# Kernel optimization log

Hardware: AMD Instinct MI355X
Metric: run time of the kernel (lower is better)

## Reference

```python
import jax, jax.numpy as jnp
import numpy as np

N = 50000   # nodes
E = 500000  # edges
NEG_SLOPE = 0.2


def _edge_softmax(e, dst, n):
    # softmax over edges grouped by destination node (DGL edge_softmax)
    m = jax.ops.segment_max(e, dst, num_segments=n)          # [N,H]
    ex = jnp.exp(e - m[dst])
    s = jax.ops.segment_sum(ex, dst, num_segments=n)
    return ex / s[dst]


def _gat(h, W, al, ar, b, src, dst, heads, d, Wres=None, act=True):
    # DGL GATConv (eval mode, no dropout)
    n = h.shape[0]
    feat = (h @ W).reshape(n, heads, d)                      # [N,H,D]
    el = jnp.sum(feat * al[None], axis=-1)                   # [N,H]
    er = jnp.sum(feat * ar[None], axis=-1)                   # [N,H]
    e = jax.nn.leaky_relu(el[src] + er[dst], NEG_SLOPE)      # [E,H]
    a = _edge_softmax(e, dst, n)                             # [E,H]
    rst = jax.ops.segment_sum(feat[src] * a[..., None], dst, num_segments=n)  # [N,H,D]
    if Wres is not None:
        res = (h @ Wres).reshape(n, heads, d)
    else:
        res = h.reshape(n, heads, d)                         # identity residual (in == heads*d)
    rst = rst + res + b.reshape(1, heads, d)
    if act:
        rst = jax.nn.elu(rst)
    return rst.reshape(n, heads * d)


def _bn(x, g, b, m, v):
    # BatchNorm1d in eval mode
    return (x - m) * g * jax.lax.rsqrt(v + 1e-5) + b


def setup_inputs() -> dict:
    key = jax.random.key(0)
    ks = jax.random.split(key, 40)
    rn = lambda i, s: jax.random.normal(ks[i], s, jnp.float32) * 0.1
    inp = dict(
        node_feats=jax.random.normal(ks[0], (N, 128), jnp.float32),
        edge_feats=jax.random.normal(ks[1], (E, 64), jnp.float32),
        src=jax.random.randint(ks[2], (E,), 0, N, jnp.int32),
        dst=jax.random.randint(ks[3], (E,), 0, N, jnp.int32),
        # GAT layer 0: 128 -> 8 heads x 16
        W0=rn(4, (128, 128)), al0=rn(5, (8, 16)), ar0=rn(6, (8, 16)), b0=rn(7, (128,)),
        g0=1.0 + rn(8, (128,)), bt0=rn(9, (128,)), m0=rn(10, (128,)),
        v0=1.0 + 0.1 * jax.random.uniform(ks[11], (128,), jnp.float32),
        # GAT layer 1: 128 -> 8 heads x 8 (residual projection)
        W1=rn(12, (128, 64)), al1=rn(13, (8, 8)), ar1=rn(14, (8, 8)), b1=rn(15, (64,)),
        Wres1=rn(16, (128, 64)),
        g1=1.0 + rn(17, (64,)), bt1=rn(18, (64,)), m1=rn(19, (64,)),
        v1=1.0 + 0.1 * jax.random.uniform(ks[20], (64,), jnp.float32),
        # GAT layer 2: 64 -> 1 head x 32 (residual projection, no activation)
        W2=rn(21, (64, 32)), al2=rn(22, (1, 32)), ar2=rn(23, (1, 32)), b2=rn(24, (32,)),
        Wres2=rn(25, (64, 32)),
        g2=1.0 + rn(26, (32,)), bt2=rn(27, (32,)), m2=rn(28, (32,)),
        v2=1.0 + 0.1 * jax.random.uniform(ks[29], (32,), jnp.float32),
        # edge projection 64 -> 128
        We=rn(30, (64, 128)), be=rn(31, (128,)),
        # edge classifier: 192 -> 32 -> 16 -> 2
        Wc1=rn(32, (192, 32)), bc1=rn(33, (32,)),
        Wc2=rn(34, (32, 16)), bc2=rn(35, (16,)),
        Wc3=rn(36, (16, 2)), bc3=rn(37, (2,)),
    )
    return inp


def reference(node_feats, edge_feats, src, dst,
              W0, al0, ar0, b0, g0, bt0, m0, v0,
              W1, al1, ar1, b1, Wres1, g1, bt1, m1, v1,
              W2, al2, ar2, b2, Wres2, g2, bt2, m2, v2,
              We, be, Wc1, bc1, Wc2, bc2, Wc3, bc3):
    h = _bn(_gat(node_feats, W0, al0, ar0, b0, src, dst, 8, 16), g0, bt0, m0, v0)
    h = _bn(_gat(h, W1, al1, ar1, b1, src, dst, 8, 8, Wres1), g1, bt1, m1, v1)
    h = _bn(_gat(h, W2, al2, ar2, b2, src, dst, 1, 32, Wres2, act=False), g2, bt2, m2, v2)
    ef = jax.nn.relu(edge_feats @ We + be)                   # [E,128]
    rep = jnp.concatenate([h[src], h[dst], ef], axis=1)      # [E,192]
    z = jax.nn.relu(rep @ Wc1 + bc1)
    z = jax.nn.relu(z @ Wc2 + bc2)
    return z @ Wc3 + bc3                                     # [E,2]
```

## Files before the change

kernel.cpp:

```cpp
#include <hip/hip_runtime.h>
#include <cfloat>
#include <math.h>

#define NEG_SLOPE 0.2f

typedef short short8 __attribute__((ext_vector_type(8)));
typedef short short4v __attribute__((ext_vector_type(4)));
typedef float f32x4 __attribute__((ext_vector_type(4)));

__device__ __forceinline__ short f2bf(float x) {
    unsigned u = __float_as_uint(x);
    u += 0x7fffu + ((u >> 16) & 1u);
    return (short)(u >> 16);
}
__device__ __forceinline__ float bf2f(unsigned short s) {
    return __uint_as_float((unsigned)s << 16);
}

__device__ __forceinline__ void lds_fence() {
    __asm__ __volatile__("s_waitcnt lgkmcnt(0)" ::: "memory");
}


__global__ void count_deg_k(const int* __restrict__ dst, int* __restrict__ deg, int E) {
    int i = blockIdx.x * 256 + threadIdx.x;
    if (i < E) atomicAdd(&deg[dst[i]], 1);
}

__global__ void scan_k(const int* __restrict__ deg, int* __restrict__ off, int n) {
    __shared__ int part[1024];
    int tid = threadIdx.x;
    int chunk = (n + 1023) >> 10;
    int beg = tid * chunk;
    int end = min(beg + chunk, n);
    int s = 0;
    for (int i = beg; i < end; ++i) s += deg[i];
    part[tid] = s;
    __syncthreads();
    for (int d = 1; d < 1024; d <<= 1) {
        int v = (tid >= d) ? part[tid - d] : 0;
        __syncthreads();
        part[tid] += v;
        __syncthreads();
    }
    int run = (tid > 0) ? part[tid - 1] : 0;
    for (int i = beg; i < end; ++i) { off[i] = run; run += deg[i]; }
    if (tid == 1023) off[n] = part[1023];
}

__global__ void scatter_k(const int* __restrict__ src, const int* __restrict__ dst,
                          const int* __restrict__ off, int* __restrict__ cur,
                          int* __restrict__ srcp, int E) {
    int i = blockIdx.x * 256 + threadIdx.x;
    if (i >= E) return;
    int d = dst[i];
    int p = off[d] + atomicAdd(&cur[d], 1);
    srcp[p] = src[i];
}


__global__ void conv_w_k(const float* __restrict__ We, const float* __restrict__ Wc1p,
                         const float* __restrict__ Wc2,
                         short* __restrict__ WeTg, short* __restrict__ Wc1Tg,
                         short* __restrict__ Wc2Tg) {
    int t = blockIdx.x * 256 + threadIdx.x;
    if (t < 64 * 128) { int k = t >> 7, n = t & 127; WeTg[n * 64 + k] = f2bf(We[t]); }
    if (t < 128 * 32) { int k = t >> 5, n = t & 31; Wc1Tg[n * 128 + k] = f2bf(Wc1p[t]); }
    if (t < 32 * 16)  { int k = t >> 4, n = t & 15; Wc2Tg[n * 32 + k] = f2bf(Wc2[t]); }
}


template<int K, int OUT, bool B16>
__global__ __launch_bounds__(256) void gemm2_k(const float* __restrict__ A,
                                               const float* __restrict__ B1, float* __restrict__ C1,
                                               const float* __restrict__ B2, float* __restrict__ C2,
                                               short* __restrict__ C1b, int nrows) {
    constexpr int CPT  = (OUT >= 64) ? 8 : 4;
    constexpr int CG   = OUT / CPT;
    constexpr int TY   = 256 / CG;
    constexpr int ROWS = TY * 4;
    constexpr int KT   = (K < 32) ? K : 32;
    constexpr int KTP  = KT + 4;

    __shared__ float As[ROWS * KTP];
    __shared__ float Bs[KT * OUT];

    const float* B = blockIdx.y ? B2 : B1;
    float*       C = blockIdx.y ? C2 : C1;

    int t = threadIdx.x;
    int tx = t % CG, ty = t / CG;
    int row0 = blockIdx.x * ROWS;

    float acc[4][CPT];
#pragma unroll
    for (int r = 0; r < 4; ++r)
#pragma unroll
        for (int c = 0; c < CPT; ++c) acc[r][c] = 0.f;

    for (int k0 = 0; k0 < K; k0 += KT) {
        __syncthreads();
#pragma unroll
        for (int i = t; i < ROWS * (KT / 4); i += 256) {
            int row = i / (KT / 4), c4 = i % (KT / 4);
            float4 v = {0.f, 0.f, 0.f, 0.f};
            if (row0 + row < nrows)
                v = *(const float4*)&A[(size_t)(row0 + row) * K + k0 + c4 * 4];
            *(float4*)&As[row * KTP + c4 * 4] = v;
        }
#pragma unroll
        for (int i = t; i < KT * (OUT / 4); i += 256) {
            int k = i / (OUT / 4), c4 = i % (OUT / 4);
            *(float4*)&Bs[k * OUT + c4 * 4] = *(const float4*)&B[(size_t)(k0 + k) * OUT + c4 * 4];
        }
        __syncthreads();

#pragma unroll
        for (int kk4 = 0; kk4 < KT / 4; ++kk4) {
            float4 a4[4];
#pragma unroll
            for (int r = 0; r < 4; ++r)
                a4[r] = *(const float4*)&As[(ty * 4 + r) * KTP + kk4 * 4];
#pragma unroll
            for (int j = 0; j < 4; ++j) {
                int kk = kk4 * 4 + j;
                float4 b4[CPT / 4];
#pragma unroll
                for (int c = 0; c < CPT / 4; ++c)
                    b4[c] = *(const float4*)&Bs[kk * OUT + tx * CPT + c * 4];
#pragma unroll
                for (int r = 0; r < 4; ++r) {
                    float a = ((const float*)&a4[r])[j];
#pragma unroll
                    for (int c = 0; c < CPT / 4; ++c) {
                        acc[r][c * 4 + 0] = fmaf(a, b4[c].x, acc[r][c * 4 + 0]);
                        acc[r][c * 4 + 1] = fmaf(a, b4[c].y, acc[r][c * 4 + 1]);
                        acc[r][c * 4 + 2] = fmaf(a, b4[c].z, acc[r][c * 4 + 2]);
                        acc[r][c * 4 + 3] = fmaf(a, b4[c].w, acc[r][c * 4 + 3]);
                    }
                }
            }
        }
    }

#pragma unroll
    for (int r = 0; r < 4; ++r) {
        int row = row0 + ty * 4 + r;
        if (row < nrows) {
#pragma unroll
            for (int c = 0; c < CPT / 4; ++c) {
                float4 v = {acc[r][c * 4 + 0], acc[r][c * 4 + 1], acc[r][c * 4 + 2], acc[r][c * 4 + 3]};
                *(float4*)&C[(size_t)row * OUT + tx * CPT + c * 4] = v;
            }
            if (B16 && blockIdx.y == 0) {
                if constexpr (CPT == 8) {
                    short8 s;
#pragma unroll
                    for (int c = 0; c < 8; ++c) s[c] = f2bf(acc[r][c]);
                    *(short8*)&C1b[(size_t)row * OUT + tx * CPT] = s;
                } else {
                    short4v s;
#pragma unroll
                    for (int c = 0; c < 4; ++c) s[c] = f2bf(acc[r][c]);
                    *(short4v*)&C1b[(size_t)row * OUT + tx * CPT] = s;
                }
            }
        }
    }
}


template<int H, int D>
__global__ void elr_k(const float* __restrict__ feat, const float* __restrict__ al,
                      const float* __restrict__ ar, float* __restrict__ el,
                      float* __restrict__ er, int n) {
    int i = blockIdx.x * 256 + threadIdx.x;
    if (i >= n * H) return;
    int h = i % H;
    const float* f = feat + (size_t)(i / H) * (H * D) + h * D;
    float sl = 0.f, sr = 0.f;
#pragma unroll
    for (int d = 0; d < D; ++d) {
        sl = fmaf(f[d], al[h * D + d], sl);
        sr = fmaf(f[d], ar[h * D + d], sr);
    }
    el[i] = sl; er[i] = sr;
}


template<int H, int D, bool ACT>
__global__ __launch_bounds__(256) void gat_node2_k(
    const int* __restrict__ off, const int* __restrict__ srcp,
    const float* __restrict__ el, const float* __restrict__ er,
    const short* __restrict__ featb,
    const float* __restrict__ res, const float* __restrict__ bias,
    const float* __restrict__ bg, const float* __restrict__ bb,
    const float* __restrict__ bm, const float* __restrict__ bv,
    float* __restrict__ hout, int N) {
    constexpr int HD = H * D;
    constexpr bool PAIR = (HD > 64);
    constexpr int CH = 64 / H;
    int wv_ = threadIdx.x >> 6;
    int lane = threadIdx.x & 63;
    int n = blockIdx.x * 4 + wv_;
    if (n >= N) return;
    int beg = off[n], end = off[n + 1];

    int hh = lane % H;
    int cc = lane / H;
    float ern = er[(size_t)n * H + hh];

    int k0 = PAIR ? 2 * lane : lane;
    int h0 = k0 / D; if (h0 > H - 1) h0 = H - 1;

    float acc0 = 0.f, acc1 = 0.f, svp = 0.f;

    for (int i0 = beg; i0 < end; i0 += CH) {
        int iw = i0 + cc;
        float wv = 0.f;
        int sidx = 0;
        if (iw < end) {
            sidx = srcp[iw];
            float x = el[(size_t)sidx * H + hh] + ern;
            x = x > 0.f ? x : NEG_SLOPE * x;
            wv = __expf(x);
        }
        svp += wv;
        int lim = min(end - i0, CH);
        for (int r = 0; r < lim; ++r) {
            int sl = r * H + h0;
            float w0 = __shfl(wv, sl, 64);
            int s    = __shfl(sidx, sl, 64);
            if constexpr (PAIR) {
                ushort2 uv = *(const ushort2*)&featb[(size_t)s * HD + k0];
                acc0 = fmaf(w0, bf2f(uv.x), acc0);
                acc1 = fmaf(w0, bf2f(uv.y), acc1);
            } else {
                if (lane < HD)
                    acc0 = fmaf(w0, bf2f((unsigned short)featb[(size_t)s * HD + k0]), acc0);
            }
        }
    }
#pragma unroll
    for (int mm = H; mm < 64; mm <<= 1) svp += __shfl_xor(svp, mm, 64);
    bool has_edges = end > beg;
    float inv0 = has_edges ? 1.f / __shfl(svp, h0, 64) : 0.f;

    if constexpr (PAIR) {
        float2 rs = *(const float2*)&res[(size_t)n * HD + k0];
        float2 bi = *(const float2*)&bias[k0];
        float2 gm = *(const float2*)&bm[k0];
        float2 gv = *(const float2*)&bv[k0];
        float2 gg = *(const float2*)&bg[k0];
        float2 gb = *(const float2*)&bb[k0];
        float x0 = acc0 * inv0 + rs.x + bi.x;
        float x1 = acc1 * inv0 + rs.y + bi.y;
        if (ACT) { x0 = x0 > 0.f ? x0 : expm1f(x0); x1 = x1 > 0.f ? x1 : expm1f(x1); }
        float2 o;
        o.x = (x0 - gm.x) * (gg.x * rsqrtf(gv.x + 1e-5f)) + gb.x;
        o.y = (x1 - gm.y) * (gg.y * rsqrtf(gv.y + 1e-5f)) + gb.y;
        *(float2*)&hout[(size_t)n * HD + k0] = o;
    } else {
        if (lane < HD) {
            int k = k0;
            float x = acc0 * inv0 + res[(size_t)n * HD + k] + bias[k];
            if (ACT) x = x > 0.f ? x : expm1f(x);
            hout[(size_t)n * HD + k] = (x - bm[k]) * (bg[k] * rsqrtf(bv[k] + 1e-5f)) + bb[k];
        }
    }
}


__global__ __launch_bounds__(256) void edge_cls_k(
    const float* __restrict__ u1, const float* __restrict__ u2,
    const float* __restrict__ edf,
    const int* __restrict__ src, const int* __restrict__ dst,
    const short* __restrict__ WeTg, const float* __restrict__ be,
    const short* __restrict__ Wc1Tg, const float* __restrict__ bc1,
    const short* __restrict__ Wc2Tg, const float* __restrict__ bc2,
    const float* __restrict__ Wc3, const float* __restrict__ bc3,
    float* __restrict__ out, int E) {
    __shared__ short efA[4][16 * 136];
    __shared__ short z1A[4][16 * 40];
    __shared__ float z2A[4][16 * 20];

    int t = threadIdx.x;
    int w = t >> 6, lane = t & 63;
    int m = lane & 15, q = lane >> 4;
    short* efW = efA[w];
    short* z1W = z1A[w];
    float* z2W = z2A[w];

    int tiles = (E + 15) >> 4;
    int gw = blockIdx.x * 4 + w;
    int W  = gridDim.x * 4;

    float bc2h = bc2[m];
    float bc30 = bc3[0], bc31 = bc3[1];

    auto ldrow = [&](int tl, float4& a, float4& b, float4& c, float4& d) {
        int em = tl * 16 + m;
        const float* rp = edf + (size_t)(em < E ? em : E - 1) * 64;
        a = *(const float4*)(rp + q * 8);
        b = *(const float4*)(rp + q * 8 + 4);
        c = *(const float4*)(rp + 32 + q * 8);
        d = *(const float4*)(rp + 32 + q * 8 + 4);
    };
    auto ldu = [&](int tl, float (&ua)[2][4], float (&ub)[2][4]) {
#pragma unroll
        for (int r = 0; r < 4; ++r) {
            int e = tl * 16 + q * 4 + r;
            int ec = e < E ? e : E - 1;
            int s = src[ec], d = dst[ec];
            ua[0][r] = u1[(size_t)s * 32 + m];
            ua[1][r] = u1[(size_t)s * 32 + 16 + m];
            ub[0][r] = u2[(size_t)d * 32 + m];
            ub[1][r] = u2[(size_t)d * 32 + 16 + m];
        }
    };

    int tile = gw;
    float4 p0 = {0,0,0,0}, p1 = p0, p2 = p0, p3 = p0;
    float u1g[2][4], u2g[2][4];
    if (tile < tiles) { ldrow(tile, p0, p1, p2, p3); ldu(tile, u1g, u2g); }

    for (; tile < tiles; tile += W) {
        float4 c0 = p0, c1 = p1, c2 = p2, c3 = p3;
        int tn = tile + W;
        if (tn < tiles) ldrow(tn, p0, p1, p2, p3);

        int e0w = tile * 16;

        short8 A0, A1;
        A0[0] = f2bf(c0.x); A0[1] = f2bf(c0.y); A0[2] = f2bf(c0.z); A0[3] = f2bf(c0.w);
        A0[4] = f2bf(c1.x); A0[5] = f2bf(c1.y); A0[6] = f2bf(c1.z); A0[7] = f2bf(c1.w);
        A1[0] = f2bf(c2.x); A1[1] = f2bf(c2.y); A1[2] = f2bf(c2.z); A1[3] = f2bf(c2.w);
        A1[4] = f2bf(c3.x); A1[5] = f2bf(c3.y); A1[6] = f2bf(c3.z); A1[7] = f2bf(c3.w);

#pragma unroll
        for (int nt = 0; nt < 8; ++nt) {
            int col = nt * 16 + m;
            float bias = be[col];
            f32x4 acc = {bias, bias, bias, bias};
            short8 b0 = *(const short8*)&WeTg[col * 64 + q * 8];
            short8 b1 = *(const short8*)&WeTg[col * 64 + 32 + q * 8];
            acc = __builtin_amdgcn_mfma_f32_16x16x32_bf16(A0, b0, acc, 0, 0, 0);
            acc = __builtin_amdgcn_mfma_f32_16x16x32_bf16(A1, b1, acc, 0, 0, 0);
#pragma unroll
            for (int r = 0; r < 4; ++r)
                efW[(q * 4 + r) * 136 + col] = f2bf(fmaxf(acc[r], 0.f));
        }
        lds_fence();

        short8 Az[4];
#pragma unroll
        for (int kt = 0; kt < 4; ++kt)
            Az[kt] = *(const short8*)&efW[m * 136 + kt * 32 + q * 8];
#pragma unroll
        for (int nt = 0; nt < 2; ++nt) {
            int col = nt * 16 + m;
            float bias = bc1[col];
            f32x4 acc = {bias, bias, bias, bias};
#pragma unroll
            for (int kt = 0; kt < 4; ++kt) {
                short8 b = *(const short8*)&Wc1Tg[col * 128 + kt * 32 + q * 8];
                acc = __builtin_amdgcn_mfma_f32_16x16x32_bf16(Az[kt], b, acc, 0, 0, 0);
            }
#pragma unroll
            for (int r = 0; r < 4; ++r) {
                float z = acc[r] + u1g[nt][r] + u2g[nt][r];
                z1W[(q * 4 + r) * 40 + col] = f2bf(fmaxf(z, 0.f));
            }
        }
        lds_fence();

        if (tn < tiles) ldu(tn, u1g, u2g);

        {
            short8 Az1 = *(const short8*)&z1W[m * 40 + q * 8];
            short8 Bz  = *(const short8*)&Wc2Tg[m * 32 + q * 8];
            f32x4 acc = {bc2h, bc2h, bc2h, bc2h};
            acc = __builtin_amdgcn_mfma_f32_16x16x32_bf16(Az1, Bz, acc, 0, 0, 0);
#pragma unroll
            for (int r = 0; r < 4; ++r)
                z2W[(q * 4 + r) * 20 + m] = fmaxf(acc[r], 0.f);
        }
        lds_fence();

        if (lane < 16) {
            int e = lane;
            int eg = e0w + e;
            if (eg < E) {
                float a0 = bc30, a1 = bc31;
#pragma unroll
                for (int k = 0; k < 16; ++k) {
                    float z = z2W[e * 20 + k];
                    a0 = fmaf(z, Wc3[k * 2], a0);
                    a1 = fmaf(z, Wc3[k * 2 + 1], a1);
                }
                float2 o = {a0, a1};
                *(float2*)&out[(size_t)eg * 2] = o;
            }
        }
        lds_fence();
    }
}


extern "C" void kernel_launch(void* const* d_in, const int* in_sizes, int n_in,
                              void* d_out, int out_size, void* d_ws, size_t ws_size,
                              hipStream_t stream) {
    const float* node_feats = (const float*)d_in[0];
    const float* edge_feats = (const float*)d_in[1];
    const int*   src  = (const int*)d_in[2];
    const int*   dst  = (const int*)d_in[3];
    const float* W0   = (const float*)d_in[4];
    const float* al0  = (const float*)d_in[5];
    const float* ar0  = (const float*)d_in[6];
    const float* b0   = (const float*)d_in[7];
    const float* g0   = (const float*)d_in[8];
    const float* bt0  = (const float*)d_in[9];
    const float* m0   = (const float*)d_in[10];
    const float* v0   = (const float*)d_in[11];
    const float* W1   = (const float*)d_in[12];
    const float* al1  = (const float*)d_in[13];
    const float* ar1  = (const float*)d_in[14];
    const float* b1   = (const float*)d_in[15];
    const float* Wr1  = (const float*)d_in[16];
    const float* g1   = (const float*)d_in[17];
    const float* bt1  = (const float*)d_in[18];
    const float* m1   = (const float*)d_in[19];
    const float* v1   = (const float*)d_in[20];
    const float* W2   = (const float*)d_in[21];
    const float* al2  = (const float*)d_in[22];
    const float* ar2  = (const float*)d_in[23];
    const float* b2   = (const float*)d_in[24];
    const float* Wr2  = (const float*)d_in[25];
    const float* g2   = (const float*)d_in[26];
    const float* bt2  = (const float*)d_in[27];
    const float* v2m  = (const float*)d_in[28];
    const float* v2v  = (const float*)d_in[29];
    const float* We   = (const float*)d_in[30];
    const float* be   = (const float*)d_in[31];
    const float* Wc1  = (const float*)d_in[32];
    const float* bc1  = (const float*)d_in[33];
    const float* Wc2  = (const float*)d_in[34];
    const float* bc2  = (const float*)d_in[35];
    const float* Wc3  = (const float*)d_in[36];
    const float* bc3  = (const float*)d_in[37];
    float* out = (float*)d_out;

    const int N = in_sizes[0] / 128;
    const int E = in_sizes[2];

    char* p = (char*)d_ws;
    auto alloc = [&](size_t bytes) -> void* {
        void* r = (void*)p;
        p += (bytes + 255) & ~(size_t)255;
        return r;
    };
    int*   deg  = (int*)alloc((size_t)N * 4);
    int*   cur  = (int*)alloc((size_t)N * 4);
    int*   off  = (int*)alloc((size_t)(N + 1) * 4);
    int*   srcp = (int*)alloc((size_t)E * 4);
    float* feat = (float*)alloc((size_t)N * 128 * 4);
    short* featb= (short*)alloc((size_t)N * 128 * 2);
    float* resf = (float*)alloc((size_t)N * 64 * 4);
    float* h1   = (float*)alloc((size_t)N * 128 * 4);
    float* h2   = (float*)alloc((size_t)N * 64 * 4);
    float* h3   = (float*)alloc((size_t)N * 32 * 4);
    float* el   = (float*)alloc((size_t)N * 8 * 4);
    float* er   = (float*)alloc((size_t)N * 8 * 4);
    short* WeTg = (short*)alloc((size_t)128 * 64 * 2);
    short* Wc1Tg= (short*)alloc((size_t)32 * 128 * 2);
    short* Wc2Tg= (short*)alloc((size_t)16 * 32 * 2);
    float* u1   = h1;
    float* u2   = h1 + (size_t)N * 32;

    hipMemsetAsync(deg, 0, (size_t)N * 4, stream);
    hipMemsetAsync(cur, 0, (size_t)N * 4, stream);

    int eb = (E + 255) / 256;
    count_deg_k<<<eb, 256, 0, stream>>>(dst, deg, E);
    scan_k<<<1, 1024, 0, stream>>>(deg, off, N);
    scatter_k<<<eb, 256, 0, stream>>>(src, dst, off, cur, srcp, E);
    conv_w_k<<<32, 256, 0, stream>>>(We, Wc1 + 64 * 32, Wc2, WeTg, Wc1Tg, Wc2Tg);

    int nb4 = (N + 3) / 4;

    gemm2_k<128,128,true><<<dim3((N + 63) / 64, 1), 256, 0, stream>>>(node_feats, W0, feat, W0, resf, featb, N);
    elr_k<8,16><<<(N * 8 + 255) / 256, 256, 0, stream>>>(feat, al0, ar0, el, er, N);
    gat_node2_k<8,16,true><<<nb4, 256, 0, stream>>>(off, srcp, el, er, featb, node_feats,
                                                    b0, g0, bt0, m0, v0, h1, N);
    gemm2_k<128,64,true><<<dim3((N + 127) / 128, 2), 256, 0, stream>>>(h1, W1, feat, Wr1, resf, featb, N);
    elr_k<8,8><<<(N * 8 + 255) / 256, 256, 0, stream>>>(feat, al1, ar1, el, er, N);
    gat_node2_k<8,8,true><<<nb4, 256, 0, stream>>>(off, srcp, el, er, featb, resf,
                                                   b1, g1, bt1, m1, v1, h2, N);
    gemm2_k<64,32,true><<<dim3((N + 127) / 128, 2), 256, 0, stream>>>(h2, W2, feat, Wr2, resf, featb, N);
    elr_k<1,32><<<(N + 255) / 256, 256, 0, stream>>>(feat, al2, ar2, el, er, N);
    gat_node2_k<1,32,false><<<nb4, 256, 0, stream>>>(off, srcp, el, er, featb, resf,
                                                     b2, g2, bt2, v2m, v2v, h3, N);
    gemm2_k<32,32,false><<<dim3((N + 127) / 128, 2), 256, 0, stream>>>(h3, Wc1, u1, Wc1 + 32 * 32, u2, nullptr, N);
    edge_cls_k<<<1024, 256, 0, stream>>>(u1, u2, edge_feats, src, dst,
                                         WeTg, be, Wc1Tg, bc1,
                                         Wc2Tg, bc2, Wc3, bc3, out, E);
}
```

Baseline: 669.7 us.

## Switch node GEMMs to bf16 MFMA, store hidden states as bf16, parallelize scan

Replaces the fp32 LDS-tiled SIMT node GEMMs with a bf16 MFMA kernel that reads pre-transposed bf16 weights converted once in an expanded conv_w kernel. Hidden activations h1/h2/h3 and the attention features are now kept in bf16, which halves node-side traffic, and el/er are computed from the bf16 features. The single-block degree scan is split into three kernels so more threads work in parallel. The edge classifier now hoists bias loads and loads the u1/u2 gathers in place instead of prefetching them. This adds bf16 rounding error on the residual projections and intermediate states, which may affect accuracy.

```diff
diff --git a/kernel.cpp b/kernel.cpp
--- a/kernel.cpp
+++ b/kernel.cpp
@@ -5,7 +5,6 @@
 #define NEG_SLOPE 0.2f
 
 typedef short short8 __attribute__((ext_vector_type(8)));
-typedef short short4v __attribute__((ext_vector_type(4)));
 typedef float f32x4 __attribute__((ext_vector_type(4)));
 
 __device__ __forceinline__ short f2bf(float x) {
@@ -27,14 +26,22 @@
     if (i < E) atomicAdd(&deg[dst[i]], 1);
 }
 
-__global__ void scan_k(const int* __restrict__ deg, int* __restrict__ off, int n) {
+__global__ void scanA_k(const int* __restrict__ deg, int* __restrict__ csum, int n) {
+    int t = blockIdx.x * 256 + threadIdx.x;
+    int ch = (n + 4095) >> 12;
+    int beg = t * ch, end = min(beg + ch, n);
+    int s = 0;
+    for (int i = beg; i < end; ++i) s += deg[i];
+    csum[t] = s;
+}
+
+__global__ void scanB_k(int* __restrict__ csum) {
     __shared__ int part[1024];
     int tid = threadIdx.x;
-    int chunk = (n + 1023) >> 10;
-    int beg = tid * chunk;
-    int end = min(beg + chunk, n);
+    int c[4];
     int s = 0;
-    for (int i = beg; i < end; ++i) s += deg[i];
+#pragma unroll
+    for (int i = 0; i < 4; ++i) { c[i] = csum[tid * 4 + i]; s += c[i]; }
     part[tid] = s;
     __syncthreads();
     for (int d = 1; d < 1024; d <<= 1) {
@@ -43,9 +50,19 @@
         part[tid] += v;
         __syncthreads();
     }
-    int run = (tid > 0) ? part[tid - 1] : 0;
+    int base = (tid > 0) ? part[tid - 1] : 0;
+#pragma unroll
+    for (int i = 0; i < 4; ++i) { csum[tid * 4 + i] = base; base += c[i]; }
+}
+
+__global__ void scanC_k(const int* __restrict__ deg, const int* __restrict__ csum,
+                        int* __restrict__ off, int n, int E) {
+    int t = blockIdx.x * 256 + threadIdx.x;
+    int ch = (n + 4095) >> 12;
+    int beg = t * ch, end = min(beg + ch, n);
+    int run = csum[t];
     for (int i = beg; i < end; ++i) { off[i] = run; run += deg[i]; }
-    if (tid == 1023) off[n] = part[1023];
+    if (t == 0) off[n] = E;
 }
 
 __global__ void scatter_k(const int* __restrict__ src, const int* __restrict__ dst,
@@ -59,111 +76,97 @@
 }
 
 
-__global__ void conv_w_k(const float* __restrict__ We, const float* __restrict__ Wc1p,
-                         const float* __restrict__ Wc2,
-                         short* __restrict__ WeTg, short* __restrict__ Wc1Tg,
-                         short* __restrict__ Wc2Tg) {
+struct WSec { const float* src; short* dst; int K, OUT, base; };
+
+__global__ void conv_w_k(const float* W0, const float* W1, const float* Wr1,
+                         const float* W2, const float* Wr2, const float* Wc1,
+                         const float* We, const float* Wc2,
+                         short* W0T, short* W1T, short* Wr1T, short* W2T, short* Wr2T,
+                         short* Wc1aT, short* Wc1bT, short* WeT, short* Wc1T, short* Wc2T) {
     int t = blockIdx.x * 256 + threadIdx.x;
-    if (t < 64 * 128) { int k = t >> 7, n = t & 127; WeTg[n * 64 + k] = f2bf(We[t]); }
-    if (t < 128 * 32) { int k = t >> 5, n = t & 31; Wc1Tg[n * 128 + k] = f2bf(Wc1p[t]); }
-    if (t < 32 * 16)  { int k = t >> 4, n = t & 15; Wc2Tg[n * 32 + k] = f2bf(Wc2[t]); }
-}
-
-
-template<int K, int OUT, bool B16>
-__global__ __launch_bounds__(256) void gemm2_k(const float* __restrict__ A,
-                                               const float* __restrict__ B1, float* __restrict__ C1,
-                                               const float* __restrict__ B2, float* __restrict__ C2,
-                                               short* __restrict__ C1b, int nrows) {
-    constexpr int CPT  = (OUT >= 64) ? 8 : 4;
-    constexpr int CG   = OUT / CPT;
-    constexpr int TY   = 256 / CG;
-    constexpr int ROWS = TY * 4;
-    constexpr int KT   = (K < 32) ? K : 32;
-    constexpr int KTP  = KT + 4;
-
-    __shared__ float As[ROWS * KTP];
-    __shared__ float Bs[KT * OUT];
-
-    const float* B = blockIdx.y ? B2 : B1;
-    float*       C = blockIdx.y ? C2 : C1;
-
-    int t = threadIdx.x;
-    int tx = t % CG, ty = t / CG;
-    int row0 = blockIdx.x * ROWS;
-
-    float acc[4][CPT];
-#pragma unroll
-    for (int r = 0; r < 4; ++r)
-#pragma unroll
-        for (int c = 0; c < CPT; ++c) acc[r][c] = 0.f;
-
-    for (int k0 = 0; k0 < K; k0 += KT) {
-        __syncthreads();
-#pragma unroll
-        for (int i = t; i < ROWS * (KT / 4); i += 256) {
-            int row = i / (KT / 4), c4 = i % (KT / 4);
-            float4 v = {0.f, 0.f, 0.f, 0.f};
-            if (row0 + row < nrows)
-                v = *(const float4*)&A[(size_t)(row0 + row) * K + k0 + c4 * 4];
-            *(float4*)&As[row * KTP + c4 * 4] = v;
-        }
-#pragma unroll
-        for (int i = t; i < KT * (OUT / 4); i += 256) {
-            int k = i / (OUT / 4), c4 = i % (OUT / 4);
-            *(float4*)&Bs[k * OUT + c4 * 4] = *(const float4*)&B[(size_t)(k0 + k) * OUT + c4 * 4];
-        }
-        __syncthreads();
-
-#pragma unroll
-        for (int kk4 = 0; kk4 < KT / 4; ++kk4) {
-            float4 a4[4];
-#pragma unroll
-            for (int r = 0; r < 4; ++r)
-                a4[r] = *(const float4*)&As[(ty * 4 + r) * KTP + kk4 * 4];
-#pragma unroll
-            for (int j = 0; j < 4; ++j) {
-                int kk = kk4 * 4 + j;
-                float4 b4[CPT / 4];
-#pragma unroll
-                for (int c = 0; c < CPT / 4; ++c)
-                    b4[c] = *(const float4*)&Bs[kk * OUT + tx * CPT + c * 4];
-#pragma unroll
-                for (int r = 0; r < 4; ++r) {
-                    float a = ((const float*)&a4[r])[j];
-#pragma unroll
-                    for (int c = 0; c < CPT / 4; ++c) {
-                        acc[r][c * 4 + 0] = fmaf(a, b4[c].x, acc[r][c * 4 + 0]);
-                        acc[r][c * 4 + 1] = fmaf(a, b4[c].y, acc[r][c * 4 + 1]);
-                        acc[r][c * 4 + 2] = fmaf(a, b4[c].z, acc[r][c * 4 + 2]);
-                        acc[r][c * 4 + 3] = fmaf(a, b4[c].w, acc[r][c * 4 + 3]);
-                    }
-                }
-            }
-        }
-    }
-
-#pragma unroll
-    for (int r = 0; r < 4; ++r) {
-        int row = row0 + ty * 4 + r;
-        if (row < nrows) {
-#pragma unroll
-            for (int c = 0; c < CPT / 4; ++c) {
-                float4 v = {acc[r][c * 4 + 0], acc[r][c * 4 + 1], acc[r][c * 4 + 2], acc[r][c * 4 + 3]};
-                *(float4*)&C[(size_t)row * OUT + tx * CPT + c * 4] = v;
-            }
-            if (B16 && blockIdx.y == 0) {
-                if constexpr (CPT == 8) {
-                    short8 s;
-#pragma unroll
-                    for (int c = 0; c < 8; ++c) s[c] = f2bf(acc[r][c]);
-                    *(short8*)&C1b[(size_t)row * OUT + tx * CPT] = s;
-                } else {
-                    short4v s;
-#pragma unroll
-                    for (int c = 0; c < 4; ++c) s[c] = f2bf(acc[r][c]);
-                    *(short4v*)&C1b[(size_t)row * OUT + tx * CPT] = s;
-                }
+    const float* src; short* dst; int K, OUT, base;
+    if      (t < 16384) { src = W0;            dst = W0T;   K = 128; OUT = 128; base = 0; }
+    else if (t < 24576) { src = W1;            dst = W1T;   K = 128; OUT = 64;  base = 16384; }
+    else if (t < 32768) { src = Wr1;           dst = Wr1T;  K = 128; OUT = 64;  base = 24576; }
+    else if (t < 34816) { src = W2;            dst = W2T;   K = 64;  OUT = 32;  base = 32768; }
+    else if (t < 36864) { src = Wr2;           dst = Wr2T;  K = 64;  OUT = 32;  base = 34816; }
+    else if (t < 37888) { src = Wc1;           dst = Wc1aT; K = 32;  OUT = 32;  base = 36864; }
+    else if (t < 38912) { src = Wc1 + 1024;    dst = Wc1bT; K = 32;  OUT = 32;  base = 37888; }
+    else if (t < 47104) { src = We;            dst = WeT;   K = 64;  OUT = 128; base = 38912; }
+    else if (t < 51200) { src = Wc1 + 64 * 32; dst = Wc1T;  K = 128; OUT = 32;  base = 47104; }
+    else if (t < 51712) { src = Wc2;           dst = Wc2T;  K = 32;  OUT = 16;  base = 51200; }
+    else return;
+    int local = t - base;
+    int k = local / OUT, n = local % OUT;
+    dst[n * K + k] = f2bf(src[k * OUT + n]);
+}
+
+
+template<int K, int NT1, int NT2, bool C1B16, bool AF32>
+__global__ __launch_bounds__(256) void gemmM_k(const void* __restrict__ A,
+                                               const short* __restrict__ B1T, void* __restrict__ C1,
+                                               const short* __restrict__ B2T, float* __restrict__ C2,
+                                               int N) {
+    int w = threadIdx.x >> 6, lane = threadIdx.x & 63;
+    int tile = blockIdx.x * 4 + w;
+    int row0 = tile * 16;
+    if (row0 >= N) return;
+    int m = lane & 15, q = lane >> 4;
+    int arow = row0 + m; if (arow >= N) arow = N - 1;
+
+    constexpr int KT = K / 32;
+    short8 Af[KT];
+    if constexpr (AF32) {
+        const float* Ap = (const float*)A + (size_t)arow * K;
+#pragma unroll
+        for (int kt = 0; kt < KT; ++kt) {
+            float4 x = *(const float4*)&Ap[kt * 32 + q * 8];
+            float4 y = *(const float4*)&Ap[kt * 32 + q * 8 + 4];
+            short8 s;
+            s[0] = f2bf(x.x); s[1] = f2bf(x.y); s[2] = f2bf(x.z); s[3] = f2bf(x.w);
+            s[4] = f2bf(y.x); s[5] = f2bf(y.y); s[6] = f2bf(y.z); s[7] = f2bf(y.w);
+            Af[kt] = s;
+        }
+    } else {
+        const short* Ap = (const short*)A + (size_t)arow * K;
+#pragma unroll
+        for (int kt = 0; kt < KT; ++kt)
+            Af[kt] = *(const short8*)&Ap[kt * 32 + q * 8];
+    }
+
+#pragma unroll
+    for (int nt = 0; nt < NT1; ++nt) {
+        f32x4 acc = {0.f, 0.f, 0.f, 0.f};
+#pragma unroll
+        for (int kt = 0; kt < KT; ++kt) {
+            short8 b = *(const short8*)&B1T[(size_t)(nt * 16 + m) * K + kt * 32 + q * 8];
+            acc = __builtin_amdgcn_mfma_f32_16x16x32_bf16(Af[kt], b, acc, 0, 0, 0);
+        }
+#pragma unroll
+        for (int r = 0; r < 4; ++r) {
+            int row = row0 + q * 4 + r;
+            if (row < N) {
+                if constexpr (C1B16)
+                    ((short*)C1)[(size_t)row * (NT1 * 16) + nt * 16 + m] = f2bf(acc[r]);
+                else
+                    ((float*)C1)[(size_t)row * (NT1 * 16) + nt * 16 + m] = acc[r];
+            }
+        }
+    }
+    if constexpr (NT2 > 0) {
+#pragma unroll
+        for (int nt = 0; nt < NT2; ++nt) {
+            f32x4 acc = {0.f, 0.f, 0.f, 0.f};
+#pragma unroll
+            for (int kt = 0; kt < KT; ++kt) {
+                short8 b = *(const short8*)&B2T[(size_t)(nt * 16 + m) * K + kt * 32 + q * 8];
+                acc = __builtin_amdgcn_mfma_f32_16x16x32_bf16(Af[kt], b, acc, 0, 0, 0);
+            }
+#pragma unroll
+            for (int r = 0; r < 4; ++r) {
+                int row = row0 + q * 4 + r;
+                if (row < N)
+                    C2[(size_t)row * (NT2 * 16) + nt * 16 + m] = acc[r];
             }
         }
     }
@@ -171,18 +174,19 @@
 
 
 template<int H, int D>
-__global__ void elr_k(const float* __restrict__ feat, const float* __restrict__ al,
+__global__ void elr_k(const short* __restrict__ featb, const float* __restrict__ al,
                       const float* __restrict__ ar, float* __restrict__ el,
                       float* __restrict__ er, int n) {
     int i = blockIdx.x * 256 + threadIdx.x;
     if (i >= n * H) return;
     int h = i % H;
-    const float* f = feat + (size_t)(i / H) * (H * D) + h * D;
+    const short* f = featb + (size_t)(i / H) * (H * D) + h * D;
     float sl = 0.f, sr = 0.f;
 #pragma unroll
     for (int d = 0; d < D; ++d) {
-        sl = fmaf(f[d], al[h * D + d], sl);
-        sr = fmaf(f[d], ar[h * D + d], sr);
+        float v = bf2f((unsigned short)f[d]);
+        sl = fmaf(v, al[h * D + d], sl);
+        sr = fmaf(v, ar[h * D + d], sr);
     }
     el[i] = sl; er[i] = sr;
 }
@@ -196,7 +200,7 @@
     const float* __restrict__ res, const float* __restrict__ bias,
     const float* __restrict__ bg, const float* __restrict__ bb,
     const float* __restrict__ bm, const float* __restrict__ bv,
-    float* __restrict__ hout, int N) {
+    short* __restrict__ houtb, int N) {
     constexpr int HD = H * D;
     constexpr bool PAIR = (HD > 64);
     constexpr int CH = 64 / H;
@@ -256,16 +260,19 @@
         float x0 = acc0 * inv0 + rs.x + bi.x;
         float x1 = acc1 * inv0 + rs.y + bi.y;
         if (ACT) { x0 = x0 > 0.f ? x0 : expm1f(x0); x1 = x1 > 0.f ? x1 : expm1f(x1); }
-        float2 o;
-        o.x = (x0 - gm.x) * (gg.x * rsqrtf(gv.x + 1e-5f)) + gb.x;
-        o.y = (x1 - gm.y) * (gg.y * rsqrtf(gv.y + 1e-5f)) + gb.y;
-        *(float2*)&hout[(size_t)n * HD + k0] = o;
+        float o0 = (x0 - gm.x) * (gg.x * rsqrtf(gv.x + 1e-5f)) + gb.x;
+        float o1 = (x1 - gm.y) * (gg.y * rsqrtf(gv.y + 1e-5f)) + gb.y;
+        ushort2 hb;
+        hb.x = (unsigned short)f2bf(o0);
+        hb.y = (unsigned short)f2bf(o1);
+        *(ushort2*)&houtb[(size_t)n * HD + k0] = hb;
     } else {
         if (lane < HD) {
             int k = k0;
             float x = acc0 * inv0 + res[(size_t)n * HD + k] + bias[k];
             if (ACT) x = x > 0.f ? x : expm1f(x);
-            hout[(size_t)n * HD + k] = (x - bm[k]) * (bg[k] * rsqrtf(bv[k] + 1e-5f)) + bb[k];
+            float o = (x - bm[k]) * (bg[k] * rsqrtf(bv[k] + 1e-5f)) + bb[k];
+            houtb[(size_t)n * HD + k] = f2bf(o);
         }
     }
 }
@@ -295,6 +302,10 @@
     int gw = blockIdx.x * 4 + w;
     int W  = gridDim.x * 4;
 
+    float beh[8];
+#pragma unroll
+    for (int nt = 0; nt < 8; ++nt) beh[nt] = be[nt * 16 + m];
+    float bc1h0 = bc1[m], bc1h1 = bc1[16 + m];
     float bc2h = bc2[m];
     float bc30 = bc3[0], bc31 = bc3[1];
 
@@ -306,23 +317,10 @@
         c = *(const float4*)(rp + 32 + q * 8);
         d = *(const float4*)(rp + 32 + q * 8 + 4);
     };
-    auto ldu = [&](int tl, float (&ua)[2][4], float (&ub)[2][4]) {
-#pragma unroll
-        for (int r = 0; r < 4; ++r) {
-            int e = tl * 16 + q * 4 + r;
-            int ec = e < E ? e : E - 1;
-            int s = src[ec], d = dst[ec];
-            ua[0][r] = u1[(size_t)s * 32 + m];
-            ua[1][r] = u1[(size_t)s * 32 + 16 + m];
-            ub[0][r] = u2[(size_t)d * 32 + m];
-            ub[1][r] = u2[(size_t)d * 32 + 16 + m];
-        }
-    };
 
     int tile = gw;
     float4 p0 = {0,0,0,0}, p1 = p0, p2 = p0, p3 = p0;
-    float u1g[2][4], u2g[2][4];
-    if (tile < tiles) { ldrow(tile, p0, p1, p2, p3); ldu(tile, u1g, u2g); }
+    if (tile < tiles) ldrow(tile, p0, p1, p2, p3);
 
     for (; tile < tiles; tile += W) {
         float4 c0 = p0, c1 = p1, c2 = p2, c3 = p3;
@@ -330,6 +328,18 @@
         if (tn < tiles) ldrow(tn, p0, p1, p2, p3);
 
         int e0w = tile * 16;
+
+        float u1g[2][4], u2g[2][4];
+#pragma unroll
+        for (int r = 0; r < 4; ++r) {
+            int e = e0w + q * 4 + r;
+            int ec = e < E ? e : E - 1;
+            int s = src[ec], d = dst[ec];
+            u1g[0][r] = u1[(size_t)s * 32 + m];
+            u1g[1][r] = u1[(size_t)s * 32 + 16 + m];
+            u2g[0][r] = u2[(size_t)d * 32 + m];
+            u2g[1][r] = u2[(size_t)d * 32 + 16 + m];
+        }
 
         short8 A0, A1;
         A0[0] = f2bf(c0.x); A0[1] = f2bf(c0.y); A0[2] = f2bf(c0.z); A0[3] = f2bf(c0.w);
@@ -340,7 +350,7 @@
 #pragma unroll
         for (int nt = 0; nt < 8; ++nt) {
             int col = nt * 16 + m;
-            float bias = be[col];
+            float bias = beh[nt];
             f32x4 acc = {bias, bias, bias, bias};
             short8 b0 = *(const short8*)&WeTg[col * 64 + q * 8];
             short8 b1 = *(const short8*)&WeTg[col * 64 + 32 + q * 8];
@@ -359,7 +369,7 @@
 #pragma unroll
         for (int nt = 0; nt < 2; ++nt) {
             int col = nt * 16 + m;
-            float bias = bc1[col];
+            float bias = nt ? bc1h1 : bc1h0;
             f32x4 acc = {bias, bias, bias, bias};
 #pragma unroll
             for (int kt = 0; kt < 4; ++kt) {
@@ -373,8 +383,6 @@
             }
         }
         lds_fence();
-
-        if (tn < tiles) ldu(tn, u1g, u2g);
 
         {
             short8 Az1 = *(const short8*)&z1W[m * 40 + q * 8];
@@ -459,48 +467,60 @@
         p += (bytes + 255) & ~(size_t)255;
         return r;
     };
-    int*   deg  = (int*)alloc((size_t)N * 4);
-    int*   cur  = (int*)alloc((size_t)N * 4);
-    int*   off  = (int*)alloc((size_t)(N + 1) * 4);
-    int*   srcp = (int*)alloc((size_t)E * 4);
-    float* feat = (float*)alloc((size_t)N * 128 * 4);
-    short* featb= (short*)alloc((size_t)N * 128 * 2);
-    float* resf = (float*)alloc((size_t)N * 64 * 4);
-    float* h1   = (float*)alloc((size_t)N * 128 * 4);
-    float* h2   = (float*)alloc((size_t)N * 64 * 4);
-    float* h3   = (float*)alloc((size_t)N * 32 * 4);
-    float* el   = (float*)alloc((size_t)N * 8 * 4);
-    float* er   = (float*)alloc((size_t)N * 8 * 4);
-    short* WeTg = (short*)alloc((size_t)128 * 64 * 2);
-    short* Wc1Tg= (short*)alloc((size_t)32 * 128 * 2);
-    short* Wc2Tg= (short*)alloc((size_t)16 * 32 * 2);
-    float* u1   = h1;
-    float* u2   = h1 + (size_t)N * 32;
+    int*   deg   = (int*)alloc((size_t)N * 4);
+    int*   cur   = (int*)alloc((size_t)N * 4);
+    int*   off   = (int*)alloc((size_t)(N + 1) * 4);
+    int*   srcp  = (int*)alloc((size_t)E * 4);
+    int*   csum  = (int*)alloc(4096 * 4);
+    short* featb = (short*)alloc((size_t)N * 128 * 2);
+    short* h1b   = (short*)alloc((size_t)N * 128 * 2);
+    short* h2b   = (short*)alloc((size_t)N * 64 * 2);
+    short* h3b   = (short*)alloc((size_t)N * 32 * 2);
+    float* resf  = (float*)alloc((size_t)N * 64 * 4);
+    float* u1    = (float*)alloc((size_t)N * 32 * 4);
+    float* u2    = (float*)alloc((size_t)N * 32 * 4);
+    float* el    = (float*)alloc((size_t)N * 8 * 4);
+    float* er    = (float*)alloc((size_t)N * 8 * 4);
+    short* W0T   = (short*)alloc(128 * 128 * 2);
+    short* W1T   = (short*)alloc(64 * 128 * 2);
+    short* Wr1T  = (short*)alloc(64 * 128 * 2);
+    short* W2T   = (short*)alloc(32 * 64 * 2);
+    short* Wr2T  = (short*)alloc(32 * 64 * 2);
+    short* Wc1aT = (short*)alloc(32 * 32 * 2);
+    short* Wc1bT = (short*)alloc(32 * 32 * 2);
+    short* WeTg  = (short*)alloc(128 * 64 * 2);
+    short* Wc1Tg = (short*)alloc(32 * 128 * 2);
+    short* Wc2Tg = (short*)alloc(16 * 32 * 2);
 
     hipMemsetAsync(deg, 0, (size_t)N * 4, stream);
     hipMemsetAsync(cur, 0, (size_t)N * 4, stream);
 
     int eb = (E + 255) / 256;
     count_deg_k<<<eb, 256, 0, stream>>>(dst, deg, E);
-    scan_k<<<1, 1024, 0, stream>>>(deg, off, N);
+    scanA_k<<<16, 256, 0, stream>>>(deg, csum, N);
+    scanB_k<<<1, 1024, 0, stream>>>(csum);
+    scanC_k<<<16, 256, 0, stream>>>(deg, csum, off, N, E);
     scatter_k<<<eb, 256, 0, stream>>>(src, dst, off, cur, srcp, E);
-    conv_w_k<<<32, 256, 0, stream>>>(We, Wc1 + 64 * 32, Wc2, WeTg, Wc1Tg, Wc2Tg);
+    conv_w_k<<<202, 256, 0, stream>>>(W0, W1, Wr1, W2, Wr2, Wc1, We, Wc2,
+                                      W0T, W1T, Wr1T, W2T, Wr2T,
+                                      Wc1aT, Wc1bT, WeTg, Wc1Tg, Wc2Tg);
 
     int nb4 = (N + 3) / 4;
-
-    gemm2_k<128,128,true><<<dim3((N + 63) / 64, 1), 256, 0, stream>>>(node_feats, W0, feat, W0, resf, featb, N);
-    elr_k<8,16><<<(N * 8 + 255) / 256, 256, 0, stream>>>(feat, al0, ar0, el, er, N);
-    gat_node2_k<8,16,true><<<nb4, 256, 0, stream>>>(off, srcp, el, er, featb, node_feats,
-                                                    b0, g0, bt0, m0, v0, h1, N);
-    gemm2_k<128,64,true><<<dim3((N + 127) / 128, 2), 256, 0, stream>>>(h1, W1, feat, Wr1, resf, featb, N);
-    elr_k<8,8><<<(N * 8 + 255) / 256, 256, 0, stream>>>(feat, al1, ar1, el, er, N);
-    gat_node2_k<8,8,true><<<nb4, 256, 0, stream>>>(off, srcp, el, er, featb, resf,
-                                                   b1, g1, bt1, m1, v1, h2, N);
-    gemm2_k<64,32,true><<<dim3((N + 127) / 128, 2), 256, 0, stream>>>(h2, W2, feat, Wr2, resf, featb, N);
-    elr_k<1,32><<<(N + 255) / 256, 256, 0, stream>>>(feat, al2, ar2, el, er, N);
-    gat_node2_k<1,32,false><<<nb4, 256, 0, stream>>>(off, srcp, el, er, featb, resf,
-                                                     b2, g2, bt2, v2m, v2v, h3, N);
-    gemm2_k<32,32,false><<<dim3((N + 127) / 128, 2), 256, 0, stream>>>(h3, Wc1, u1, Wc1 + 32 * 32, u2, nullptr, N);
+    int gtb = ((N + 15) / 16 + 3) / 4;
+
+    gemmM_k<128, 8, 0, true, true><<<gtb, 256, 0, stream>>>(node_feats, W0T, featb, nullptr, nullptr, N);
+    elr_k<8, 16><<<(N * 8 + 255) / 256, 256, 0, stream>>>(featb, al0, ar0, el, er, N);
+    gat_node2_k<8, 16, true><<<nb4, 256, 0, stream>>>(off, srcp, el, er, featb, node_feats,
+                                                      b0, g0, bt0, m0, v0, h1b, N);
+    gemmM_k<128, 4, 4, true, false><<<gtb, 256, 0, stream>>>(h1b, W1T, featb, Wr1T, resf, N);
+    elr_k<8, 8><<<(N * 8 + 255) / 256, 256, 0, stream>>>(featb, al1, ar1, el, er, N);
+    gat_node2_k<8, 8, true><<<nb4, 256, 0, stream>>>(off, srcp, el, er, featb, resf,
+                                                     b1, g1, bt1, m1, v1, h2b, N);
+    gemmM_k<64, 2, 2, true, false><<<gtb, 256, 0, stream>>>(h2b, W2T, featb, Wr2T, resf, N);
+    elr_k<1, 32><<<(N + 255) / 256, 256, 0, stream>>>(featb, al2, ar2, el, er, N);
+    gat_node2_k<1, 32, false><<<nb4, 256, 0, stream>>>(off, srcp, el, er, featb, resf,
+                                                       b2, g2, bt2, v2m, v2v, h3b, N);
+    gemmM_k<32, 2, 2, false, false><<<gtb, 256, 0, stream>>>(h3b, Wc1aT, u1, Wc1bT, u2, N);
     edge_cls_k<<<1024, 256, 0, stream>>>(u1, u2, edge_feats, src, dst,
                                          WeTg, be, Wc1Tg, bc1,
                                          Wc2Tg, bc2, Wc3, bc3, out, E);
```

Result: faster. 577.6 us (-13.7%).
